# Optimization experiments

Hardware: AMD Instinct MI355X
Metric: run time of the kernel (lower is better)

## Reference

```python
import jax, jax.numpy as jnp
import numpy as np

B, T, D, HS = 4, 4096, 1024, 64

def setup_inputs() -> dict:
    key = jax.random.key(0)
    kx, kq, kk, kv = jax.random.split(key, 4)
    s = 1.0 / np.sqrt(D)  # torch Linear default-ish init scale
    return {
        "x": jax.random.normal(kx, (B, T, D), dtype=jnp.float32),
        "Wq": jax.random.uniform(kq, (D, HS), jnp.float32, -s, s),
        "Wk": jax.random.uniform(kk, (D, HS), jnp.float32, -s, s),
        "Wv": jax.random.uniform(kv, (D, HS), jnp.float32, -s, s),
    }

def reference(x, Wq, Wk, Wv):
    # x: [B,T,D]; Wq/Wk/Wv: [D,HS]
    q = jnp.einsum('btd,dh->bth', x, Wq)
    k = jnp.einsum('btd,dh->bth', x, Wk)
    v = jnp.einsum('btd,dh->bth', x, Wv)
    # NOTE: source scales by C**-0.5 with C = d_model (input dim), not head_size
    scale = jnp.asarray(D, x.dtype) ** -0.5
    weights = jnp.einsum('bqh,bkh->bqk', q, k) * scale  # [B,T,T]
    weights = jax.nn.softmax(weights, axis=-1)
    out = jnp.einsum('bqk,bkh->bqh', weights, v)  # [B,T,HS]
    return out
```

## Files before the change

### kernel.cpp

```cpp
#include <hip/hip_runtime.h>


typedef __bf16 bf16;
typedef __bf16 bf16x4 __attribute__((ext_vector_type(4)));
typedef __bf16 bf16x8 __attribute__((ext_vector_type(8)));
typedef float  f32x16 __attribute__((ext_vector_type(16)));

#define MFMA(a, b, c) __builtin_amdgcn_mfma_f32_32x32x16_bf16(a, b, c, 0, 0, 0)

constexpr int T = 4096, D = 1024, HS = 64;
constexpr int ROWS = 4 * T;
constexpr float QSCL = 0.045084220027797f;

__device__ __forceinline__ void gld16(const void* g, void* l) {
    __builtin_amdgcn_global_load_lds(
        (const __attribute__((address_space(1))) unsigned int*)g,
        (__attribute__((address_space(3))) unsigned int*)l, 16, 0, 0);
}

__device__ inline f32x16 zero16() {
    f32x16 z;
#pragma unroll
    for (int i = 0; i < 16; ++i) z[i] = 0.f;
    return z;
}

__global__ __launch_bounds__(256) void prep_wt(
    const float* __restrict__ Wq, const float* __restrict__ Wk,
    const float* __restrict__ Wv, bf16* __restrict__ Wt)
{
    __shared__ float Xf[64 * 68];
    const int m = blockIdx.x >> 4, dt = blockIdx.x & 15;
    const float* W = (m == 0) ? Wq : ((m == 1) ? Wk : Wv);
    const int d0 = dt * 64;
#pragma unroll
    for (int j = 0; j < 4; ++j) {
        int i = threadIdx.x + 256 * j;
        int dr = i >> 4, c4 = i & 15;
        float4 v = *(const float4*)(W + (size_t)(d0 + dr) * 64 + c4 * 4);
        *(float4*)&Xf[dr * 68 + c4 * 4] = v;
    }
    __syncthreads();
    const float scl = (m == 0) ? QSCL : 1.0f;
#pragma unroll
    for (int j = 0; j < 4; ++j) {
        int o = threadIdx.x + 256 * j;
        int h = o >> 4, dc = o & 15;
        bf16x4 w;
#pragma unroll
        for (int k = 0; k < 4; ++k) w[k] = (bf16)(Xf[(dc * 4 + k) * 68 + h] * scl);
        *(bf16x4*)(Wt + (size_t)(m * 64 + h) * D + d0 + dc * 4) = w;
    }
}

__global__ __launch_bounds__(256, 3) void qkv_proj(
    const float* __restrict__ x, const bf16* __restrict__ Wt,
    bf16* __restrict__ Qg, bf16* __restrict__ Kgt, bf16* __restrict__ Vgt)
{
    __shared__ __align__(16) float Xs[2][64 * 64];
    __shared__ __align__(16) short Ws[2][64 * 64];
    const int tid = threadIdx.x;
    const int w = tid >> 6, lane = tid & 63, ln5 = lane & 31, hi = lane >> 5;
    const int tt = w & 1, hh = w >> 1;
    const int xcd = blockIdx.x & 7, t3 = blockIdx.x >> 3;
    const int which = t3 % 3, mlocal = t3 / 3;
    const int r0 = (xcd * 32 + mlocal) * 64;
    const int wb = tid & 448;

    auto stage = [&](int kc, int buf) {
#pragma unroll
        for (int k2 = 0; k2 < 4; ++k2) {
            int s = k2 * 256 + tid;
            int r = s >> 4, j = s & 15, u = j ^ (r & 15);
            gld16(x + (size_t)(r0 + r) * D + kc * 64 + u * 4,
                  &Xs[buf][(k2 * 256 + wb) * 4]);
        }
#pragma unroll
        for (int k2 = 0; k2 < 2; ++k2) {
            int s = k2 * 256 + tid;
            int h = s >> 3, j = s & 7, u = j ^ (h & 7);
            gld16(Wt + (size_t)(which * 64 + h) * D + kc * 64 + u * 8,
                  &Ws[buf][(k2 * 256 + wb) * 8]);
        }
    };

    f32x16 acc = zero16();
    const int rx = tt * 32 + ln5;
    const int hq = hh * 32 + ln5;
    const int swz = ln5 & 7;

    stage(0, 0);
    __syncthreads();
    for (int kc = 0; kc < 16; ++kc) {
        const int cur = kc & 1;
        if (kc < 15) stage(kc + 1, cur ^ 1);
        const float* Xb = &Xs[cur][0];
        const short* Wb = &Ws[cur][0];
#pragma unroll
        for (int ks = 0; ks < 4; ++ks) {
            int u0 = ks * 4 + hi * 2;
            float4 a = *(const float4*)&Xb[rx * 64 + ((u0)     ^ (rx & 15)) * 4];
            float4 b = *(const float4*)&Xb[rx * 64 + ((u0 + 1) ^ (rx & 15)) * 4];
            bf16x8 fx;
            fx[0] = (bf16)a.x; fx[1] = (bf16)a.y; fx[2] = (bf16)a.z; fx[3] = (bf16)a.w;
            fx[4] = (bf16)b.x; fx[5] = (bf16)b.y; fx[6] = (bf16)b.z; fx[7] = (bf16)b.w;
            bf16x8 wf = *(const bf16x8*)&Wb[hq * 64 + (((ks * 2 + hi) ^ swz) * 8)];
            if (which < 2) acc = MFMA(wf, fx, acc);
            else           acc = MFMA(fx, wf, acc);
        }
        __syncthreads();
    }

    if (which < 2) {
        int t = r0 + tt * 32 + ln5;
#pragma unroll
        for (int g = 0; g < 4; ++g) {
            int h0 = hh * 32 + 8 * g + 4 * hi;
            bf16x4 v;
#pragma unroll
            for (int k = 0; k < 4; ++k) v[k] = (bf16)acc[4 * g + k];
            if (which == 0) {
                *(bf16x4*)(Qg + (size_t)t * HS + h0) = v;
            } else {
                int j = (h0 >> 3) ^ (t & 7);
                *(bf16x4*)(Kgt + (size_t)t * HS + j * 8 + 4 * hi) = v;
            }
        }
    } else {
        int hr = hh * 32 + ln5;
#pragma unroll
        for (int g = 0; g < 4; ++g) {
            int t0 = tt * 32 + 8 * g + 4 * hi;
            bf16x4 v;
#pragma unroll
            for (int k = 0; k < 4; ++k) v[k] = (bf16)acc[4 * g + k];
            int j = (t0 >> 3) ^ (hr & 7);
            *(bf16x4*)(Vgt + (size_t)r0 * HS + hr * 64 + j * 8 + 4 * hi) = v;
        }
    }
}

__global__ __launch_bounds__(256, 2) void attn(
    const bf16* __restrict__ Qg, const bf16* __restrict__ Kgt,
    const bf16* __restrict__ Vgt, float* __restrict__ Op,
    float* __restrict__ Lp, float* __restrict__ out, int split)
{
    __shared__ __align__(16) short KV[2][8192];
    __shared__ __align__(16) short Ps[4][64 * 40];
    __shared__ float Lx[128];

    const int tid = threadIdx.x;
    const int w = tid >> 6, lane = tid & 63, ln5 = lane & 31, hi = lane >> 5;
    const int wq = w & 1, wk = w >> 1;
    const int wb = tid & 448;

    int b, qt, half;
    if (split == 4) {
        int rest = blockIdx.x >> 3; qt = rest & 31;
        int combo = (blockIdx.x & 7) + 8 * (rest >> 5);
        b = combo >> 2; half = combo & 3;
    } else if (split == 2) {
        int c2 = blockIdx.x & 7; b = c2 >> 1; half = c2 & 1; qt = blockIdx.x >> 3;
    } else { b = blockIdx.x & 3; half = 0; qt = blockIdx.x >> 2; }

    const int rbase = b * T;
    const int seg = T / split;
    const int kb0 = rbase + half * seg;
    const int nc = seg / 64;
    const int qrow0 = rbase + qt * 128 + wq * 64;

    bf16x8 bq[2][4];
    {
        const bf16* qp = Qg + (size_t)(qrow0 + ln5) * HS + hi * 8;
#pragma unroll
        for (int qs = 0; qs < 2; ++qs)
#pragma unroll
            for (int ks = 0; ks < 4; ++ks)
                bq[qs][ks] = *(const bf16x8*)(qp + (size_t)qs * 32 * HS + ks * 16);
    }

    const bf16* Kc = Kgt + (size_t)kb0 * HS;
    const bf16* Vc = Vgt + (size_t)kb0 * HS;
    auto stage = [&](int c, int buf) {
#pragma unroll
        for (int k2 = 0; k2 < 2; ++k2) {
            int s = k2 * 256 + tid;
            gld16(Kc + (size_t)c * 4096 + s * 8, &KV[buf][(k2 * 256 + wb) * 8]);
            gld16(Vc + (size_t)c * 4096 + s * 8, &KV[buf][4096 + (k2 * 256 + wb) * 8]);
        }
    };

    f32x16 O00 = zero16(), O01 = zero16(), O10 = zero16(), O11 = zero16();
    float l0 = 0.f, l1 = 0.f;
    short* Pw = &Ps[w][0];
    const int swz = ln5 & 7;
    const int krow = (wk * 32 + ln5) * 64;

    stage(0, 0);
    __syncthreads();

    for (int c = 0; c < nc; ++c) {
        const int cur = c & 1;
        if (c + 1 < nc) stage(c + 1, cur ^ 1);
        const short* Kb = &KV[cur][0];
        const short* Vb = &KV[cur][4096];

        f32x16 S0 = zero16(), S1 = zero16();
#pragma unroll
        for (int ks = 0; ks < 4; ++ks) {
            bf16x8 kf = *(const bf16x8*)&Kb[krow + (((ks * 2 + hi) ^ swz) * 8)];
            S0 = MFMA(kf, bq[0][ks], S0);
            S1 = MFMA(kf, bq[1][ks], S1);
        }

#pragma unroll
        for (int g = 0; g < 4; ++g) {
            float p0 = __builtin_amdgcn_exp2f(S0[4 * g + 0]);
            float p1 = __builtin_amdgcn_exp2f(S0[4 * g + 1]);
            float p2 = __builtin_amdgcn_exp2f(S0[4 * g + 2]);
            float p3 = __builtin_amdgcn_exp2f(S0[4 * g + 3]);
            l0 += (p0 + p1) + (p2 + p3);
            bf16x4 pv; pv[0] = (bf16)p0; pv[1] = (bf16)p1; pv[2] = (bf16)p2; pv[3] = (bf16)p3;
            *(bf16x4*)&Pw[ln5 * 40 + 8 * g + 4 * hi] = pv;
        }
#pragma unroll
        for (int g = 0; g < 4; ++g) {
            float p0 = __builtin_amdgcn_exp2f(S1[4 * g + 0]);
            float p1 = __builtin_amdgcn_exp2f(S1[4 * g + 1]);
            float p2 = __builtin_amdgcn_exp2f(S1[4 * g + 2]);
            float p3 = __builtin_amdgcn_exp2f(S1[4 * g + 3]);
            l1 += (p0 + p1) + (p2 + p3);
            bf16x4 pv; pv[0] = (bf16)p0; pv[1] = (bf16)p1; pv[2] = (bf16)p2; pv[3] = (bf16)p3;
            *(bf16x4*)&Pw[(32 + ln5) * 40 + 8 * g + 4 * hi] = pv;
        }

#pragma unroll
        for (int ks = 0; ks < 2; ++ks) {
            int ku = (wk * 4 + ks * 2 + hi) ^ swz;
            bf16x8 pf0 = *(const bf16x8*)&Pw[ln5 * 40 + ks * 16 + hi * 8];
            bf16x8 pf1 = *(const bf16x8*)&Pw[(32 + ln5) * 40 + ks * 16 + hi * 8];
            bf16x8 vf0 = *(const bf16x8*)&Vb[ln5 * 64 + ku * 8];
            bf16x8 vf1 = *(const bf16x8*)&Vb[(32 + ln5) * 64 + ku * 8];
            O00 = MFMA(vf0, pf0, O00);
            O01 = MFMA(vf0, pf1, O01);
            O10 = MFMA(vf1, pf0, O10);
            O11 = MFMA(vf1, pf1, O11);
        }
        __syncthreads();
    }

    l0 += __shfl_xor(l0, 32, 64);
    l1 += __shfl_xor(l1, 32, 64);

    float* Ox = (float*)&KV[0][0];
    if (wk == 1) {
#pragma unroll
        for (int g = 0; g < 4; ++g)
#pragma unroll
            for (int k = 0; k < 4; ++k) {
                int h0 = 8 * g + 4 * hi + k;
                Ox[wq * 4096 + h0 * 64 + ln5]             = O00[4 * g + k];
                Ox[wq * 4096 + h0 * 64 + 32 + ln5]        = O01[4 * g + k];
                Ox[wq * 4096 + (32 + h0) * 64 + ln5]      = O10[4 * g + k];
                Ox[wq * 4096 + (32 + h0) * 64 + 32 + ln5] = O11[4 * g + k];
            }
        if (hi == 0) { Lx[wq * 64 + ln5] = l0; Lx[wq * 64 + 32 + ln5] = l1; }
    }
    __syncthreads();
    if (wk == 0) {
#pragma unroll
        for (int g = 0; g < 4; ++g)
#pragma unroll
            for (int k = 0; k < 4; ++k) {
                int h0 = 8 * g + 4 * hi + k;
                O00[4 * g + k] += Ox[wq * 4096 + h0 * 64 + ln5];
                O01[4 * g + k] += Ox[wq * 4096 + h0 * 64 + 32 + ln5];
                O10[4 * g + k] += Ox[wq * 4096 + (32 + h0) * 64 + ln5];
                O11[4 * g + k] += Ox[wq * 4096 + (32 + h0) * 64 + 32 + ln5];
            }
        l0 += Lx[wq * 64 + ln5];
        l1 += Lx[wq * 64 + 32 + ln5];

        int q0 = qrow0 + ln5, q1 = qrow0 + 32 + ln5;
        if (split == 1) {
            float i0 = 1.0f / l0, i1 = 1.0f / l1;
#pragma unroll
            for (int g = 0; g < 4; ++g) {
                int h0 = 8 * g + 4 * hi;
                float4 o;
                o.x = O00[4*g+0]*i0; o.y = O00[4*g+1]*i0; o.z = O00[4*g+2]*i0; o.w = O00[4*g+3]*i0;
                *(float4*)(out + (size_t)q0 * HS + h0) = o;
                o.x = O01[4*g+0]*i1; o.y = O01[4*g+1]*i1; o.z = O01[4*g+2]*i1; o.w = O01[4*g+3]*i1;
                *(float4*)(out + (size_t)q1 * HS + h0) = o;
                o.x = O10[4*g+0]*i0; o.y = O10[4*g+1]*i0; o.z = O10[4*g+2]*i0; o.w = O10[4*g+3]*i0;
                *(float4*)(out + (size_t)q0 * HS + 32 + h0) = o;
                o.x = O11[4*g+0]*i1; o.y = O11[4*g+1]*i1; o.z = O11[4*g+2]*i1; o.w = O11[4*g+3]*i1;
                *(float4*)(out + (size_t)q1 * HS + 32 + h0) = o;
            }
        } else {
            float* Od = Op + (size_t)half * ROWS * HS;
#pragma unroll
            for (int g = 0; g < 4; ++g) {
                int h0 = 8 * g + 4 * hi;
                float4 o;
                o.x = O00[4*g+0]; o.y = O00[4*g+1]; o.z = O00[4*g+2]; o.w = O00[4*g+3];
                *(float4*)(Od + (size_t)q0 * HS + h0) = o;
                o.x = O01[4*g+0]; o.y = O01[4*g+1]; o.z = O01[4*g+2]; o.w = O01[4*g+3];
                *(float4*)(Od + (size_t)q1 * HS + h0) = o;
                o.x = O10[4*g+0]; o.y = O10[4*g+1]; o.z = O10[4*g+2]; o.w = O10[4*g+3];
                *(float4*)(Od + (size_t)q0 * HS + 32 + h0) = o;
                o.x = O11[4*g+0]; o.y = O11[4*g+1]; o.z = O11[4*g+2]; o.w = O11[4*g+3];
                *(float4*)(Od + (size_t)q1 * HS + 32 + h0) = o;
            }
            if (hi == 0) {
                Lp[half * ROWS + q0] = l0;
                Lp[half * ROWS + q1] = l1;
            }
        }
    }
}

__global__ __launch_bounds__(256) void attn_reduce(
    const float* __restrict__ Op, const float* __restrict__ Lp,
    float* __restrict__ out, int split)
{
    int idx = blockIdx.x * 256 + threadIdx.x;
    int row = idx >> 4;
    float4 s; s.x = s.y = s.z = s.w = 0.f;
    float lsum = 0.f;
    for (int h = 0; h < split; ++h) {
        float4 a = *(const float4*)(Op + (size_t)h * ROWS * HS + (size_t)idx * 4);
        s.x += a.x; s.y += a.y; s.z += a.z; s.w += a.w;
        lsum += Lp[h * ROWS + row];
    }
    float inv = 1.0f / lsum;
    s.x *= inv; s.y *= inv; s.z *= inv; s.w *= inv;
    *(float4*)(out + (size_t)idx * 4) = s;
}

extern "C" void kernel_launch(void* const* d_in, const int* in_sizes, int n_in,
                              void* d_out, int out_size, void* d_ws, size_t ws_size,
                              hipStream_t stream)
{
    const float* x  = (const float*)d_in[0];
    const float* Wq = (const float*)d_in[1];
    const float* Wk = (const float*)d_in[2];
    const float* Wv = (const float*)d_in[3];
    float* out = (float*)d_out;

    char* ws = (char*)d_ws;
    bf16* Qg  = (bf16*)(ws);
    bf16* Kgt = (bf16*)(ws + ((size_t)2 << 20));
    bf16* Vgt = (bf16*)(ws + ((size_t)4 << 20));
    bf16* Wt  = (bf16*)(ws + ((size_t)6 << 20));
    float* Lp = (float*)(ws + ((size_t)6 << 20));
    float* Op = (float*)(ws + ((size_t)6 << 20) + ((size_t)1 << 19));

    const size_t base = ((size_t)6 << 20) + ((size_t)1 << 19);
    int split = 1;
    if (ws_size >= base + (size_t)4 * ROWS * HS * sizeof(float)) split = 4;
    else if (ws_size >= base + (size_t)2 * ROWS * HS * sizeof(float)) split = 2;

    prep_wt<<<48, 256, 0, stream>>>(Wq, Wk, Wv, Wt);
    qkv_proj<<<768, 256, 0, stream>>>(x, Wt, Qg, Kgt, Vgt);
    attn<<<128 * split, 256, 0, stream>>>(Qg, Kgt, Vgt, Op, Lp, out, split);
    if (split > 1)
        attn_reduce<<<(ROWS * HS / 4) / 256, 256, 0, stream>>>(Op, Lp, out, split);
}
```

Baseline: 151.7 us.

## Load K/V fragments directly from global into registers, drop LDS staging

Removes the double-buffered LDS staging of K and V chunks and its per-iteration block barrier. Each wave now loads its MFMA K fragments straight from global memory into registers, prefetching the next chunk's K, and loads V fragments at the start of each iteration. LDS is kept only for the per-wave P tile and the final reduction, which shrinks shared memory use and removes the __syncthreads in the main loop. The cost is redundant global/L2 traffic, since the two waves sharing a K/V chunk each fetch it separately, and the V loads sit exposed inside the iteration with no prefetch.

```diff
diff --git a/kernel.cpp b/kernel.cpp
--- a/kernel.cpp
+++ b/kernel.cpp
@@ -145,14 +145,12 @@
     const bf16* __restrict__ Vgt, float* __restrict__ Op,
     float* __restrict__ Lp, float* __restrict__ out, int split)
 {
-    __shared__ __align__(16) short KV[2][8192];
-    __shared__ __align__(16) short Ps[4][64 * 40];
+    __shared__ __align__(16) short PO[16384];
     __shared__ float Lx[128];
 
     const int tid = threadIdx.x;
     const int w = tid >> 6, lane = tid & 63, ln5 = lane & 31, hi = lane >> 5;
     const int wq = w & 1, wk = w >> 1;
-    const int wb = tid & 448;
 
     int b, qt, half;
     if (split == 4) {
@@ -181,37 +179,46 @@
 
     const bf16* Kc = Kgt + (size_t)kb0 * HS;
     const bf16* Vc = Vgt + (size_t)kb0 * HS;
-    auto stage = [&](int c, int buf) {
-#pragma unroll
-        for (int k2 = 0; k2 < 2; ++k2) {
-            int s = k2 * 256 + tid;
-            gld16(Kc + (size_t)c * 4096 + s * 8, &KV[buf][(k2 * 256 + wb) * 8]);
-            gld16(Vc + (size_t)c * 4096 + s * 8, &KV[buf][4096 + (k2 * 256 + wb) * 8]);
-        }
-    };
 
     f32x16 O00 = zero16(), O01 = zero16(), O10 = zero16(), O11 = zero16();
     float l0 = 0.f, l1 = 0.f;
-    short* Pw = &Ps[w][0];
+    short* Pw = &PO[w * 2560];
     const int swz = ln5 & 7;
     const int krow = (wk * 32 + ln5) * 64;
-
-    stage(0, 0);
-    __syncthreads();
+    const int ko0 = krow + ((0 + hi) ^ swz) * 8;
+    const int ko1 = krow + ((2 + hi) ^ swz) * 8;
+    const int ko2 = krow + ((4 + hi) ^ swz) * 8;
+    const int ko3 = krow + ((6 + hi) ^ swz) * 8;
+    const int ku0 = ((wk * 4 + 0 + hi) ^ swz) * 8;
+    const int ku1 = ((wk * 4 + 2 + hi) ^ swz) * 8;
+    const int vr0 = ln5 * 64, vr1 = (32 + ln5) * 64;
+
+    bf16x8 kf0 = *(const bf16x8*)(Kc + ko0);
+    bf16x8 kf1 = *(const bf16x8*)(Kc + ko1);
+    bf16x8 kf2 = *(const bf16x8*)(Kc + ko2);
+    bf16x8 kf3 = *(const bf16x8*)(Kc + ko3);
 
     for (int c = 0; c < nc; ++c) {
-        const int cur = c & 1;
-        if (c + 1 < nc) stage(c + 1, cur ^ 1);
-        const short* Kb = &KV[cur][0];
-        const short* Vb = &KV[cur][4096];
+        const bf16* Vb = Vc + (size_t)c * 4096;
+        bf16x8 v00 = *(const bf16x8*)(Vb + vr0 + ku0);
+        bf16x8 v01 = *(const bf16x8*)(Vb + vr0 + ku1);
+        bf16x8 v10 = *(const bf16x8*)(Vb + vr1 + ku0);
+        bf16x8 v11 = *(const bf16x8*)(Vb + vr1 + ku1);
+        const bool pf = (c + 1 < nc);
+        bf16x8 kn0, kn1, kn2, kn3;
+        if (pf) {
+            const bf16* Kn = Kc + (size_t)(c + 1) * 4096;
+            kn0 = *(const bf16x8*)(Kn + ko0);
+            kn1 = *(const bf16x8*)(Kn + ko1);
+            kn2 = *(const bf16x8*)(Kn + ko2);
+            kn3 = *(const bf16x8*)(Kn + ko3);
+        }
 
         f32x16 S0 = zero16(), S1 = zero16();
-#pragma unroll
-        for (int ks = 0; ks < 4; ++ks) {
-            bf16x8 kf = *(const bf16x8*)&Kb[krow + (((ks * 2 + hi) ^ swz) * 8)];
-            S0 = MFMA(kf, bq[0][ks], S0);
-            S1 = MFMA(kf, bq[1][ks], S1);
-        }
+        S0 = MFMA(kf0, bq[0][0], S0); S1 = MFMA(kf0, bq[1][0], S1);
+        S0 = MFMA(kf1, bq[0][1], S0); S1 = MFMA(kf1, bq[1][1], S1);
+        S0 = MFMA(kf2, bq[0][2], S0); S1 = MFMA(kf2, bq[1][2], S1);
+        S0 = MFMA(kf3, bq[0][3], S0); S1 = MFMA(kf3, bq[1][3], S1);
 
 #pragma unroll
         for (int g = 0; g < 4; ++g) {
@@ -234,25 +241,29 @@
             *(bf16x4*)&Pw[(32 + ln5) * 40 + 8 * g + 4 * hi] = pv;
         }
 
-#pragma unroll
-        for (int ks = 0; ks < 2; ++ks) {
-            int ku = (wk * 4 + ks * 2 + hi) ^ swz;
-            bf16x8 pf0 = *(const bf16x8*)&Pw[ln5 * 40 + ks * 16 + hi * 8];
-            bf16x8 pf1 = *(const bf16x8*)&Pw[(32 + ln5) * 40 + ks * 16 + hi * 8];
-            bf16x8 vf0 = *(const bf16x8*)&Vb[ln5 * 64 + ku * 8];
-            bf16x8 vf1 = *(const bf16x8*)&Vb[(32 + ln5) * 64 + ku * 8];
-            O00 = MFMA(vf0, pf0, O00);
-            O01 = MFMA(vf0, pf1, O01);
-            O10 = MFMA(vf1, pf0, O10);
-            O11 = MFMA(vf1, pf1, O11);
-        }
-        __syncthreads();
+        {
+            bf16x8 pf0 = *(const bf16x8*)&Pw[ln5 * 40 + hi * 8];
+            bf16x8 pf1 = *(const bf16x8*)&Pw[(32 + ln5) * 40 + hi * 8];
+            O00 = MFMA(v00, pf0, O00);
+            O01 = MFMA(v00, pf1, O01);
+            O10 = MFMA(v10, pf0, O10);
+            O11 = MFMA(v10, pf1, O11);
+            pf0 = *(const bf16x8*)&Pw[ln5 * 40 + 16 + hi * 8];
+            pf1 = *(const bf16x8*)&Pw[(32 + ln5) * 40 + 16 + hi * 8];
+            O00 = MFMA(v01, pf0, O00);
+            O01 = MFMA(v01, pf1, O01);
+            O10 = MFMA(v11, pf0, O10);
+            O11 = MFMA(v11, pf1, O11);
+        }
+
+        if (pf) { kf0 = kn0; kf1 = kn1; kf2 = kn2; kf3 = kn3; }
     }
 
     l0 += __shfl_xor(l0, 32, 64);
     l1 += __shfl_xor(l1, 32, 64);
 
-    float* Ox = (float*)&KV[0][0];
+    __syncthreads();
+    float* Ox = (float*)&PO[0];
     if (wk == 1) {
 #pragma unroll
         for (int g = 0; g < 4; ++g)
```

Result: faster. 147.8 us (-2.6%).
